# Optimization experiments

Measured on AMD Instinct MI355X. Metric: run time of the kernel, lower is better.

The kernel has to match this reference:

```python
import jax, jax.numpy as jnp
import numpy as np

B, S, HID = 4, 2048, 768
H, DBLK, HD = 12, 256, 64  # heads, block_dim = HID//3, head_dim


def setup_inputs() -> dict:
    key = jax.random.key(0)
    ks = jax.random.split(key, 7)
    scale = 0.02
    return {
        "inputs": jax.random.normal(ks[0], (B, S, HID), jnp.float32),
        "Wq": jax.random.normal(ks[1], (H, DBLK, HD), jnp.float32) * scale,
        "bq": jax.random.normal(ks[2], (H, HD), jnp.float32) * scale,
        "Wk": jax.random.normal(ks[3], (H, DBLK, HD), jnp.float32) * scale,
        "bk": jax.random.normal(ks[4], (H, HD), jnp.float32) * scale,
        "Wv": jax.random.normal(ks[5], (H, DBLK, HD), jnp.float32) * scale,
        "bv": jax.random.normal(ks[6], (H, HD), jnp.float32) * scale,
    }


def reference(inputs, Wq, bq, Wk, bk, Wv, bv):
    b, s, hid = inputs.shape
    h, dblk, hd = Wq.shape
    hpm = h // 3  # heads per modality
    # split hidden into 3 modality blocks: [B, S, 3, DBLK]
    xm = inputs.reshape(b, s, 3, dblk)

    def proj(W, bias):
        # block-diagonal GEMM: each modality's x projected by its hpm heads
        y = jnp.einsum('bsmd,mhde->bmhse', xm, W.reshape(3, hpm, dblk, hd))
        y = y + bias.reshape(3, hpm, 1, hd)
        return y.reshape(b, h, s, hd)

    Q = proj(Wq, bq)
    K = proj(Wk, bk)
    V = proj(Wv, bv)

    scores = jnp.einsum('bhse,bhte->bhst', Q, K) / jnp.sqrt(jnp.float32(hd))
    probs = jax.nn.softmax(scores, axis=-1)  # dropout p=0 -> identity
    ctx = jnp.einsum('bhst,bhte->bhse', probs, V)
    # concat heads along feature dim: [B, S, H*HD]
    return ctx.transpose(0, 2, 1, 3).reshape(b, s, h * hd)
```

## Files before the change

kernel.cpp:

```cpp
#include <hip/hip_runtime.h>
#include <hip/hip_bf16.h>

#define B_    4
#define S_    2048
#define HID_  768
#define H_    12
#define DBLK_ 256
#define HD_   64
#define BH_   (B_ * H_)
#define QSZ_  (B_ * H_ * S_ * HD_)
#define WTSZ_ (3 * H_ * HD_ * DBLK_)

typedef _Float16 f16x4 __attribute__((ext_vector_type(4)));
typedef _Float16 f16x8 __attribute__((ext_vector_type(8)));
typedef float    f32x4 __attribute__((ext_vector_type(4)));

#if __has_builtin(__builtin_amdgcn_exp2f)
#define EXP2(x) __builtin_amdgcn_exp2f(x)
#else
#define EXP2(x) exp2f(x)
#endif

__global__ __launch_bounds__(256) void wconv(
    const float* __restrict__ Wq, const float* __restrict__ Wk,
    const float* __restrict__ Wv, _Float16* __restrict__ whf)
{
    const int idx  = blockIdx.x * 256 + threadIdx.x;
    const int j    = idx & 7;
    const int lane = (idx >> 3) & 63;
    const int et   = (idx >> 9) & 1;
    const int kk   = (idx >> 10) & 7;
    const int eh   = (idx >> 13) & 1;
    const int ph   = idx >> 14;
    const int h    = ph % H_;
    const int p    = ph / H_;
    const int e = eh * 32 + et * 16 + (lane & 15);
    const int k = kk * 32 + (lane >> 4) * 8 + j;
    const float* W = (p == 0) ? Wq : (p == 1) ? Wk : Wv;
    whf[idx] = (_Float16)W[((size_t)h * DBLK_ + k) * HD_ + e];
}

__global__ __launch_bounds__(256, 3) void qkv_proj(
    const float* __restrict__ x, const _Float16* __restrict__ whf,
    const float* __restrict__ bq, const float* __restrict__ bk,
    const float* __restrict__ bv,
    _Float16* __restrict__ qo, _Float16* __restrict__ khf,
    _Float16* __restrict__ vtf)
{
    const int i   = blockIdx.x;
    const int g   = i >> 7;
    const int sc  = i & 127;
    const int m   = g >> 1;
    const int s0g = sc * 64;

    const int tid  = threadIdx.x;
    const int lane = tid & 63;
    const int w    = tid >> 6;
    const int ln   = lane & 15;
    const int qd   = lane >> 4;
    const int h    = 2 * g + (w >> 1);
    const int eh   = w & 1;

    __shared__ _Float16 xs[64 * 256];

    {
        const int rr   = tid >> 6;
        const int c4   = tid & 63;
        const int g16  = c4 >> 1;
        const int half = c4 & 1;
        #pragma unroll
        for (int pass = 0; pass < 16; pass++) {
            const int r = pass * 4 + rr;
            const float4 v = *(const float4*)(
                x + (size_t)(s0g + r) * HID_ + m * DBLK_ + c4 * 4);
            f16x4 hv;
            hv[0] = (_Float16)v.x; hv[1] = (_Float16)v.y;
            hv[2] = (_Float16)v.z; hv[3] = (_Float16)v.w;
            *(f16x4*)(xs + r * 256 + ((g16 ^ (r & 7)) * 8) + half * 4) = hv;
        }
    }
    __syncthreads();

    f32x4 acc[3][2][4];
    #pragma unroll
    for (int p = 0; p < 3; p++)
        #pragma unroll
        for (int et = 0; et < 2; et++)
            #pragma unroll
            for (int st = 0; st < 4; st++)
                acc[p][et][st] = (f32x4){0.f, 0.f, 0.f, 0.f};

    const _Float16* wb = whf + (size_t)((h * 2 + eh) * 16) * 512 + lane * 8;

    for (int kk = 0; kk < 8; kk++) {
        f16x8 a[4];
        #pragma unroll
        for (int st = 0; st < 4; st++)
            a[st] = *(const f16x8*)(
                xs + (st * 16 + ln) * 256 + (((kk * 4 + qd) ^ (ln & 7)) * 8));
        #pragma unroll
        for (int p = 0; p < 3; p++)
            #pragma unroll
            for (int et = 0; et < 2; et++) {
                const f16x8 bb = *(const f16x8*)(
                    wb + (size_t)p * 196608 + (kk * 2 + et) * 512);
                #pragma unroll
                for (int st = 0; st < 4; st++)
                    acc[p][et][st] = __builtin_amdgcn_mfma_f32_16x16x32_f16(
                        a[st], bb, acc[p][et][st], 0, 0, 0);
            }
    }

    const float QS = 0.18033688011112042f;
    const int b    = s0g >> 11;
    const int s0   = s0g & 2047;
    const int bhh  = b * H_ + h;
    const int tile = s0 >> 6;

    #pragma unroll
    for (int et = 0; et < 2; et++) {
        const int e = eh * 32 + et * 16 + ln;
        const float biasq = bq[h * HD_ + e];
        const float biask = bk[h * HD_ + e];
        const float biasv = bv[h * HD_ + e];
        #pragma unroll
        for (int st = 0; st < 4; st++) {
            #pragma unroll
            for (int r = 0; r < 4; r++) {
                const int sl = st * 16 + qd * 4 + r;
                qo[((size_t)bhh * S_ + s0 + sl) * HD_ + e] =
                    (_Float16)((acc[0][et][st][r] + biasq) * QS);
                khf[((size_t)bhh * 32 + tile) * 4096 + sl * 64 + e] =
                    (_Float16)(acc[1][et][st][r] + biask);
            }
            f16x4 vv;
            #pragma unroll
            for (int r = 0; r < 4; r++) vv[r] = (_Float16)(acc[2][et][st][r] + biasv);
            *(f16x4*)(vtf + (((size_t)bhh * 32 + tile) * 4 + st) * 1024
                          + e * 16 + qd * 4) = vv;
        }
    }
}

__global__ __launch_bounds__(256, 3) void attn(
    const _Float16* __restrict__ qh, const _Float16* __restrict__ khf,
    const _Float16* __restrict__ vtf, float* __restrict__ out)
{
    const int i    = blockIdx.x;
    const int slot = i >> 3;
    const int bh   = (i & 7) * 6 + (slot % 6);
    const int qt   = slot / 6;
    const int h = bh % H_, b = bh / H_;
    const int q0 = qt * 64;

    const int tid  = threadIdx.x;
    const int lane = tid & 63;
    const int w    = tid >> 6;
    const int ln   = lane & 15;
    const int qd   = lane >> 4;

    __shared__ f32x4 cbuf[16 * 64];
    __shared__ float l_sh[4][4][16];

    f16x8 qf[4][2];
    #pragma unroll
    for (int st = 0; st < 4; st++) {
        const _Float16* qb = qh + ((size_t)bh * S_ + q0 + st * 16 + ln) * HD_;
        qf[st][0] = *(const f16x8*)(qb + qd * 8);
        qf[st][1] = *(const f16x8*)(qb + 32 + qd * 8);
    }

    f32x4 o[4][4];
    float lr[4];
    #pragma unroll
    for (int st = 0; st < 4; st++) {
        lr[st] = 0.f;
        #pragma unroll
        for (int dn = 0; dn < 4; dn++) o[st][dn] = (f32x4){0.f, 0.f, 0.f, 0.f};
    }

    const _Float16* kb  = khf + (size_t)bh * 32 * 4096 + (w * 16 + ln) * 64 + qd * 8;
    const _Float16* vbp = vtf + ((size_t)bh * 128 + w) * 1024 + ln * 16 + qd * 4;

    f16x8 kc[2], kn[2];
    f16x4 vc[4], vn[4];
    kc[0] = *(const f16x8*)(kb);
    kc[1] = *(const f16x8*)(kb + 32);
    #pragma unroll
    for (int dn = 0; dn < 4; dn++) vc[dn] = *(const f16x4*)(vbp + dn * 256);

    auto body = [&](int it, f16x8 (&kcur)[2], f16x8 (&knxt)[2],
                    f16x4 (&vcur)[4], f16x4 (&vnxt)[4]) {
        const size_t nb = (size_t)((it < 31) ? it + 1 : it) * 4096;
        knxt[0] = *(const f16x8*)(kb + nb);
        knxt[1] = *(const f16x8*)(kb + nb + 32);
        #pragma unroll
        for (int dn = 0; dn < 4; dn++)
            vnxt[dn] = *(const f16x4*)(vbp + nb + dn * 256);

        #pragma unroll
        for (int st = 0; st < 4; st++) {
            f32x4 s = (f32x4){0.f, 0.f, 0.f, 0.f};
            s = __builtin_amdgcn_mfma_f32_16x16x32_f16(kcur[0], qf[st][0], s, 0, 0, 0);
            s = __builtin_amdgcn_mfma_f32_16x16x32_f16(kcur[1], qf[st][1], s, 0, 0, 0);
            const float p0 = EXP2(s[0]), p1 = EXP2(s[1]);
            const float p2 = EXP2(s[2]), p3 = EXP2(s[3]);
            lr[st] += (p0 + p1) + (p2 + p3);
            f16x4 a;
            a[0] = (_Float16)p0; a[1] = (_Float16)p1;
            a[2] = (_Float16)p2; a[3] = (_Float16)p3;
            #pragma unroll
            for (int dn = 0; dn < 4; dn++)
                o[st][dn] = __builtin_amdgcn_mfma_f32_16x16x16f16(
                    a, vcur[dn], o[st][dn], 0, 0, 0);
        }
    };

    for (int it = 0; it < 32; it += 2) {
        body(it,     kc, kn, vc, vn);
        body(it + 1, kn, kc, vn, vc);
    }

    #pragma unroll
    for (int st = 0; st < 4; st++) {
        float l = lr[st];
        l += __shfl_xor(l, 16);
        l += __shfl_xor(l, 32);
        if (qd == 0) l_sh[w][st][ln] = l;
    }
    __syncthreads();
    float lt[4];
    #pragma unroll
    for (int st = 0; st < 4; st++)
        lt[st] = l_sh[0][st][ln] + l_sh[1][st][ln] + l_sh[2][st][ln] + l_sh[3][st][ln];

    for (int st = 0; st < 4; st++) {
        #pragma unroll
        for (int dn = 0; dn < 4; dn++)
            cbuf[(w * 4 + dn) * 64 + lane] = o[st][dn];
        __syncthreads();
        f32x4 fo = cbuf[(0 * 4 + w) * 64 + lane];
        fo += cbuf[(1 * 4 + w) * 64 + lane];
        fo += cbuf[(2 * 4 + w) * 64 + lane];
        fo += cbuf[(3 * 4 + w) * 64 + lane];
        float inv[4];
        #pragma unroll
        for (int r = 0; r < 4; r++)
            inv[r] = 1.f / __shfl(lt[st], qd * 4 + r, 16);
        float* op = out + ((size_t)b * S_ + q0 + st * 16 + qd * 4) * HID_
                  + (size_t)h * HD_ + w * 16 + ln;
        #pragma unroll
        for (int r = 0; r < 4; r++)
            op[(size_t)r * HID_] = fo[r] * inv[r];
        __syncthreads();
    }
}

extern "C" void kernel_launch(void* const* d_in, const int* in_sizes, int n_in,
                              void* d_out, int out_size, void* d_ws, size_t ws_size,
                              hipStream_t stream) {
    const float* x  = (const float*)d_in[0];
    const float* Wq = (const float*)d_in[1];
    const float* bq = (const float*)d_in[2];
    const float* Wk = (const float*)d_in[3];
    const float* bk = (const float*)d_in[4];
    const float* Wv = (const float*)d_in[5];
    const float* bv = (const float*)d_in[6];
    float* out = (float*)d_out;

    _Float16* q  = (_Float16*)d_ws;
    _Float16* k  = q + QSZ_;
    _Float16* vt = k + QSZ_;
    const size_t need = ((size_t)3 * QSZ_ + WTSZ_) * sizeof(_Float16);
    _Float16* wh = (ws_size >= need) ? (vt + QSZ_)
                                     : (_Float16*)d_out;

    wconv<<<WTSZ_ / 256, 256, 0, stream>>>(Wq, Wk, Wv, wh);
    qkv_proj<<<768, 256, 0, stream>>>(x, wh, bq, bk, bv, q, k, vt);
    attn<<<1536, 256, 0, stream>>>(q, k, vt, out);
}
```

Measured before the change: 196.1 us.

## Stage K/V tiles in LDS via async global_load_lds with swizzled layout

The attention kernel changes from splitting keys across waves (with a cross-wave LDS reduction) to splitting queries across waves. Each block now handles 128 queries, and K/V tiles are double-buffered in LDS through async global-to-LDS loads, so all four waves share each tile. The projection kernel writes K and V in an XOR-swizzled layout to match the LDS read pattern and avoid bank conflicts. The aim is to cut global K/V traffic and drop the final reduction, at the cost of a barrier every iteration and half as many blocks.

```diff
diff --git a/kernel.cpp b/kernel.cpp
--- a/kernel.cpp
+++ b/kernel.cpp
@@ -20,6 +20,9 @@
 #else
 #define EXP2(x) exp2f(x)
 #endif
+
+typedef const void __attribute__((address_space(1)))* gptr_t;
+typedef       void __attribute__((address_space(3)))* sptr_t;
 
 __global__ __launch_bounds__(256) void wconv(
     const float* __restrict__ Wq, const float* __restrict__ Wk,
@@ -116,28 +119,31 @@
     const int s0   = s0g & 2047;
     const int bhh  = b * H_ + h;
     const int tile = s0 >> 6;
+    const size_t tb = (size_t)(bhh * 32 + tile) * 4096;
 
     #pragma unroll
     for (int et = 0; et < 2; et++) {
-        const int e = eh * 32 + et * 16 + ln;
-        const float biasq = bq[h * HD_ + e];
-        const float biask = bk[h * HD_ + e];
-        const float biasv = bv[h * HD_ + e];
+        const int d  = eh * 32 + et * 16 + ln;
+        const int dc = d >> 3, d7 = d & 7;
+        const float biasq = bq[h * HD_ + d];
+        const float biask = bk[h * HD_ + d];
+        const float biasv = bv[h * HD_ + d];
+        const int dn = eh * 2 + et;
         #pragma unroll
         for (int st = 0; st < 4; st++) {
             #pragma unroll
             for (int r = 0; r < 4; r++) {
                 const int sl = st * 16 + qd * 4 + r;
-                qo[((size_t)bhh * S_ + s0 + sl) * HD_ + e] =
+                qo[((size_t)bhh * S_ + s0 + sl) * HD_ + d] =
                     (_Float16)((acc[0][et][st][r] + biasq) * QS);
-                khf[((size_t)bhh * 32 + tile) * 4096 + sl * 64 + e] =
+                khf[tb + sl * 64 + ((dc ^ (sl & 7)) * 8) + d7] =
                     (_Float16)(acc[1][et][st][r] + biask);
             }
             f16x4 vv;
             #pragma unroll
             for (int r = 0; r < 4; r++) vv[r] = (_Float16)(acc[2][et][st][r] + biasv);
-            *(f16x4*)(vtf + (((size_t)bhh * 32 + tile) * 4 + st) * 1024
-                          + e * 16 + qd * 4) = vv;
+            const int chunk = (qd * 2 + (st >> 1)) ^ (ln & 7);
+            *(f16x4*)(vtf + tb + dn * 1024 + ln * 64 + chunk * 8 + (st & 1) * 4) = vv;
         }
     }
 }
@@ -151,7 +157,7 @@
     const int bh   = (i & 7) * 6 + (slot % 6);
     const int qt   = slot / 6;
     const int h = bh % H_, b = bh / H_;
-    const int q0 = qt * 64;
+    const int q0 = qt * 128;
 
     const int tid  = threadIdx.x;
     const int lane = tid & 63;
@@ -159,100 +165,112 @@
     const int ln   = lane & 15;
     const int qd   = lane >> 4;
 
-    __shared__ f32x4 cbuf[16 * 64];
-    __shared__ float l_sh[4][4][16];
-
-    f16x8 qf[4][2];
-    #pragma unroll
-    for (int st = 0; st < 4; st++) {
-        const _Float16* qb = qh + ((size_t)bh * S_ + q0 + st * 16 + ln) * HD_;
+    __shared__ __align__(16) char lds[2][16384];
+
+    f16x8 qf[2][2];
+    #pragma unroll
+    for (int st = 0; st < 2; st++) {
+        const _Float16* qb = qh + ((size_t)bh * S_ + q0 + w * 32 + st * 16 + ln) * HD_;
         qf[st][0] = *(const f16x8*)(qb + qd * 8);
         qf[st][1] = *(const f16x8*)(qb + 32 + qd * 8);
     }
 
-    f32x4 o[4][4];
-    float lr[4];
-    #pragma unroll
-    for (int st = 0; st < 4; st++) {
-        lr[st] = 0.f;
+    f32x4 o[2][4];
+    float lr[2] = {0.f, 0.f};
+    #pragma unroll
+    for (int st = 0; st < 2; st++)
         #pragma unroll
         for (int dn = 0; dn < 4; dn++) o[st][dn] = (f32x4){0.f, 0.f, 0.f, 0.f};
-    }
-
-    const _Float16* kb  = khf + (size_t)bh * 32 * 4096 + (w * 16 + ln) * 64 + qd * 8;
-    const _Float16* vbp = vtf + ((size_t)bh * 128 + w) * 1024 + ln * 16 + qd * 4;
-
-    f16x8 kc[2], kn[2];
-    f16x4 vc[4], vn[4];
-    kc[0] = *(const f16x8*)(kb);
-    kc[1] = *(const f16x8*)(kb + 32);
-    #pragma unroll
-    for (int dn = 0; dn < 4; dn++) vc[dn] = *(const f16x4*)(vbp + dn * 256);
-
-    auto body = [&](int it, f16x8 (&kcur)[2], f16x8 (&knxt)[2],
-                    f16x4 (&vcur)[4], f16x4 (&vnxt)[4]) {
-        const size_t nb = (size_t)((it < 31) ? it + 1 : it) * 4096;
-        knxt[0] = *(const f16x8*)(kb + nb);
-        knxt[1] = *(const f16x8*)(kb + nb + 32);
+
+    const char* kbase = (const char*)(khf + (size_t)bh * 32 * 4096);
+    const char* vbase = (const char*)(vtf + (size_t)bh * 32 * 4096);
+    const int   seg   = w * 1024 + lane * 16;
+    const int   wseg  = w * 1024;
+
+    auto dma = [&](int it, int buf) {
+        const char* ks = kbase + (size_t)it * 8192;
+        const char* vs = vbase + (size_t)it * 8192;
+        char* lk = &lds[buf][0];
+        char* lv = &lds[buf][8192];
+        #pragma unroll
+        for (int q = 0; q < 2; q++) {
+            __builtin_amdgcn_global_load_lds(
+                (gptr_t)(ks + q * 4096 + seg), (sptr_t)(lk + q * 4096 + wseg), 16, 0, 0);
+            __builtin_amdgcn_global_load_lds(
+                (gptr_t)(vs + q * 4096 + seg), (sptr_t)(lv + q * 4096 + wseg), 16, 0, 0);
+        }
+    };
+
+    dma(0, 0);
+
+    for (int it = 0; it < 32; it++) {
+        const int buf = it & 1;
+        __syncthreads();
+        if (it + 1 < 32) dma(it + 1, buf ^ 1);
+
+        const char* lk = &lds[buf][0];
+        const char* lv = &lds[buf][8192];
+
+        f16x8 kf[4][2];
+        #pragma unroll
+        for (int mt = 0; mt < 4; mt++) {
+            kf[mt][0] = *(const f16x8*)(lk + (16 * mt + ln) * 128 + ((qd       ^ (ln & 7)) * 16));
+            kf[mt][1] = *(const f16x8*)(lk + (16 * mt + ln) * 128 + (((4 + qd) ^ (ln & 7)) * 16));
+        }
+        f16x8 v8[4][2];
         #pragma unroll
         for (int dn = 0; dn < 4; dn++)
-            vnxt[dn] = *(const f16x4*)(vbp + nb + dn * 256);
-
-        #pragma unroll
-        for (int st = 0; st < 4; st++) {
-            f32x4 s = (f32x4){0.f, 0.f, 0.f, 0.f};
-            s = __builtin_amdgcn_mfma_f32_16x16x32_f16(kcur[0], qf[st][0], s, 0, 0, 0);
-            s = __builtin_amdgcn_mfma_f32_16x16x32_f16(kcur[1], qf[st][1], s, 0, 0, 0);
-            const float p0 = EXP2(s[0]), p1 = EXP2(s[1]);
-            const float p2 = EXP2(s[2]), p3 = EXP2(s[3]);
-            lr[st] += (p0 + p1) + (p2 + p3);
-            f16x4 a;
-            a[0] = (_Float16)p0; a[1] = (_Float16)p1;
-            a[2] = (_Float16)p2; a[3] = (_Float16)p3;
+            #pragma unroll
+            for (int hf = 0; hf < 2; hf++)
+                v8[dn][hf] = *(const f16x8*)(
+                    lv + dn * 2048 + ln * 128 + (((qd * 2 + hf) ^ (ln & 7)) * 16));
+
+        #pragma unroll
+        for (int st = 0; st < 2; st++) {
+            f16x4 a[4];
+            #pragma unroll
+            for (int mt = 0; mt < 4; mt++) {
+                f32x4 s = (f32x4){0.f, 0.f, 0.f, 0.f};
+                s = __builtin_amdgcn_mfma_f32_16x16x32_f16(kf[mt][0], qf[st][0], s, 0, 0, 0);
+                s = __builtin_amdgcn_mfma_f32_16x16x32_f16(kf[mt][1], qf[st][1], s, 0, 0, 0);
+                const float p0 = EXP2(s[0]), p1 = EXP2(s[1]);
+                const float p2 = EXP2(s[2]), p3 = EXP2(s[3]);
+                lr[st] += (p0 + p1) + (p2 + p3);
+                f16x4 av;
+                av[0] = (_Float16)p0; av[1] = (_Float16)p1;
+                av[2] = (_Float16)p2; av[3] = (_Float16)p3;
+                a[mt] = av;
+            }
             #pragma unroll
             for (int dn = 0; dn < 4; dn++)
-                o[st][dn] = __builtin_amdgcn_mfma_f32_16x16x16f16(
-                    a, vcur[dn], o[st][dn], 0, 0, 0);
-        }
-    };
-
-    for (int it = 0; it < 32; it += 2) {
-        body(it,     kc, kn, vc, vn);
-        body(it + 1, kn, kc, vn, vc);
-    }
-
-    #pragma unroll
-    for (int st = 0; st < 4; st++) {
+                #pragma unroll
+                for (int c = 0; c < 4; c++) {
+                    const f16x8 vv8 = v8[dn][c >> 1];
+                    const f16x4 vv = (c & 1)
+                        ? __builtin_shufflevector(vv8, vv8, 4, 5, 6, 7)
+                        : __builtin_shufflevector(vv8, vv8, 0, 1, 2, 3);
+                    o[st][dn] = __builtin_amdgcn_mfma_f32_16x16x16f16(a[c], vv, o[st][dn], 0, 0, 0);
+                }
+        }
+    }
+
+    #pragma unroll
+    for (int st = 0; st < 2; st++) {
         float l = lr[st];
         l += __shfl_xor(l, 16);
         l += __shfl_xor(l, 32);
-        if (qd == 0) l_sh[w][st][ln] = l;
-    }
-    __syncthreads();
-    float lt[4];
-    #pragma unroll
-    for (int st = 0; st < 4; st++)
-        lt[st] = l_sh[0][st][ln] + l_sh[1][st][ln] + l_sh[2][st][ln] + l_sh[3][st][ln];
-
-    for (int st = 0; st < 4; st++) {
-        #pragma unroll
-        for (int dn = 0; dn < 4; dn++)
-            cbuf[(w * 4 + dn) * 64 + lane] = o[st][dn];
-        __syncthreads();
-        f32x4 fo = cbuf[(0 * 4 + w) * 64 + lane];
-        fo += cbuf[(1 * 4 + w) * 64 + lane];
-        fo += cbuf[(2 * 4 + w) * 64 + lane];
-        fo += cbuf[(3 * 4 + w) * 64 + lane];
         float inv[4];
         #pragma unroll
         for (int r = 0; r < 4; r++)
-            inv[r] = 1.f / __shfl(lt[st], qd * 4 + r, 16);
-        float* op = out + ((size_t)b * S_ + q0 + st * 16 + qd * 4) * HID_
-                  + (size_t)h * HD_ + w * 16 + ln;
-        #pragma unroll
-        for (int r = 0; r < 4; r++)
-            op[(size_t)r * HID_] = fo[r] * inv[r];
-        __syncthreads();
+            inv[r] = 1.f / __shfl(l, qd * 4 + r, 16);
+        #pragma unroll
+        for (int dn = 0; dn < 4; dn++) {
+            float* op = out + ((size_t)b * S_ + q0 + w * 32 + st * 16 + qd * 4) * HID_
+                      + (size_t)h * HD_ + dn * 16 + ln;
+            #pragma unroll
+            for (int r = 0; r < 4; r++)
+                op[(size_t)r * HID_] = o[st][dn][r] * inv[r];
+        }
     }
 }
 
@@ -277,5 +295,5 @@
 
     wconv<<<WTSZ_ / 256, 256, 0, stream>>>(Wq, Wk, Wv, wh);
     qkv_proj<<<768, 256, 0, stream>>>(x, wh, bq, bk, bv, q, k, vt);
-    attn<<<1536, 256, 0, stream>>>(q, k, vt, out);
-}
+    attn<<<768, 256, 0, stream>>>(q, k, vt, out);
+}
```

After: 178.2 us. 1.1x faster.
